# Kernel tuning notes

Measured on AMD Instinct MI355X. Metric: run time of the kernel, lower is better.

The kernel has to match this reference:

```python
import jax, jax.numpy as jnp
import numpy as np

N, P, D, C = 2048, 64, 512, 32   # bs*n_vars, patch_num, hidden_dim, cluster_num
H, DFF, L = 8, 2048, 3           # heads, ffn dim, encoder layers
TEMP = 10.0
EPS = 1e-10
LN_EPS = 1e-5


def setup_inputs() -> dict:
    key = jax.random.key(0)
    ks = jax.random.split(key, 18)
    s = 0.02  # small init to keep activations sane
    inp = {}
    inp["input_series"] = jax.random.normal(ks[0], (N, P, D), jnp.float32)
    pi = jax.random.uniform(ks[1], (C,), jnp.float32) + 0.1
    inp["text_pi"] = pi / pi.sum()
    A = jax.random.uniform(ks[2], (C, C), jnp.float32) + 0.1
    inp["text_A"] = A / A.sum(axis=1, keepdims=True)
    # stacked per-layer TransformerEncoderLayer params (torch post-norm, relu)
    inp["qkv_w"] = jax.random.normal(ks[3], (L, 3 * D, D), jnp.float32) * s
    inp["qkv_b"] = jnp.zeros((L, 3 * D), jnp.float32)
    inp["out_w"] = jax.random.normal(ks[4], (L, D, D), jnp.float32) * s
    inp["out_b"] = jnp.zeros((L, D), jnp.float32)
    inp["ln1_w"] = jnp.ones((L, D), jnp.float32)
    inp["ln1_b"] = jnp.zeros((L, D), jnp.float32)
    inp["ff1_w"] = jax.random.normal(ks[5], (L, DFF, D), jnp.float32) * s
    inp["ff1_b"] = jnp.zeros((L, DFF), jnp.float32)
    inp["ff2_w"] = jax.random.normal(ks[6], (L, D, DFF), jnp.float32) * s
    inp["ff2_b"] = jnp.zeros((L, D), jnp.float32)
    inp["ln2_w"] = jnp.ones((L, D), jnp.float32)
    inp["ln2_b"] = jnp.zeros((L, D), jnp.float32)
    inp["mus"] = jax.random.normal(ks[7], (C, D), jnp.float32)
    return inp


def _layer_norm(x, w, b):
    m = x.mean(axis=-1, keepdims=True)
    v = ((x - m) ** 2).mean(axis=-1, keepdims=True)
    return (x - m) * jax.lax.rsqrt(v + LN_EPS) * w + b


def _encoder_layer(x, qkv_w, qkv_b, out_w, out_b, ln1_w, ln1_b,
                   ff1_w, ff1_b, ff2_w, ff2_b, ln2_w, ln2_b):
    n, p, d = x.shape
    dh = d // H
    qkv = x @ qkv_w.T + qkv_b                       # [n,p,3d]
    q, k, v = jnp.split(qkv, 3, axis=-1)
    def split_heads(t):
        return t.reshape(n, p, H, dh).transpose(0, 2, 1, 3)  # [n,h,p,dh]
    q, k, v = split_heads(q), split_heads(k), split_heads(v)
    scores = jnp.einsum('nhqd,nhkd->nhqk', q, k) / (dh ** 0.5)
    attn = jax.nn.softmax(scores, axis=-1)
    o = jnp.einsum('nhqk,nhkd->nhqd', attn, v)
    o = o.transpose(0, 2, 1, 3).reshape(n, p, d)
    o = o @ out_w.T + out_b
    x = _layer_norm(x + o, ln1_w, ln1_b)            # post-norm
    f = jax.nn.relu(x @ ff1_w.T + ff1_b) @ ff2_w.T + ff2_b
    return _layer_norm(x + f, ln2_w, ln2_b)


def reference(input_series, text_pi, text_A, qkv_w, qkv_b, out_w, out_b,
              ln1_w, ln1_b, ff1_w, ff1_b, ff2_w, ff2_b, ln2_w, ln2_b, mus):
    x = input_series
    for l in range(L):
        x = _encoder_layer(x, qkv_w[l], qkv_b[l], out_w[l], out_b[l],
                           ln1_w[l], ln1_b[l], ff1_w[l], ff1_b[l],
                           ff2_w[l], ff2_b[l], ln2_w[l], ln2_b[l])
    emb_ts = x                                       # [N,P,D]
    # ClusterCenters: softmax of exp(-||x - tanh(mu)||^2 / T)
    mu = jnp.tanh(mus)                               # [C,D]
    dist = ((emb_ts ** 2).sum(-1)[..., None]
            + (mu ** 2).sum(-1)[None, None, :]
            - 2.0 * jnp.einsum('npd,cd->npc', emb_ts, mu))  # [N,P,C]
    z = jnp.exp(-dist / TEMP)
    logits_all = z / z.sum(axis=-1, keepdims=True)
    log_za = jnp.log(logits_all + EPS)               # [N,P,C]
    # sequential HMM-style recursion over patches
    l0 = jax.nn.softmax(jnp.log(text_pi + EPS)[None, :] + log_za[:, 0], axis=-1)
    def step(c, lz):
        c2 = jax.nn.softmax(jnp.log(c @ text_A + EPS) + lz, axis=-1)
        return c2, c2
    _, ys = jax.lax.scan(step, l0, jnp.swapaxes(log_za[:, 1:], 0, 1))  # [P-1,N,C]
    cluster_probs = jnp.concatenate([l0[:, None], jnp.swapaxes(ys, 0, 1)], axis=1)
    entropy_loss = -jnp.sum(cluster_probs * jnp.log(cluster_probs + EPS), axis=-1).mean()
    return (cluster_probs, emb_ts, text_pi, text_A, entropy_loss)
```

## Files before the change

kernel.cpp:

```cpp
#include <hip/hip_runtime.h>
#include <stdint.h>


typedef __bf16 bf16;
typedef __bf16 bf16x2 __attribute__((ext_vector_type(2)));
typedef __bf16 bf16x4 __attribute__((ext_vector_type(4)));
typedef __bf16 bf16x8 __attribute__((ext_vector_type(8)));
typedef float  f32x4  __attribute__((ext_vector_type(4)));
typedef float  f32x2  __attribute__((ext_vector_type(2)));

#define EPSF 1e-10f
#define NROWS 131072L

__device__ __forceinline__ float bflo(uint32_t u){ return __uint_as_float(u << 16); }
__device__ __forceinline__ float bfhi(uint32_t u){ return __uint_as_float(u & 0xffff0000u); }

__device__ __forceinline__ void gload_lds16(const bf16* g, bf16* l){
  __builtin_amdgcn_global_load_lds((const __attribute__((address_space(1))) uint32_t*)g,
                                   (__attribute__((address_space(3))) uint32_t*)l,
                                   16, 0, 0);
}

__global__ void k_f2bf(const float* __restrict__ in, bf16* __restrict__ out, long n){
  const long stride = (long)gridDim.x * blockDim.x * 4;
  for (long i = ((long)blockIdx.x * blockDim.x + threadIdx.x) * 4; i < n; i += stride){
    f32x4 v = *(const f32x4*)(in + i);
    bf16x4 o = { (bf16)v[0], (bf16)v[1], (bf16)v[2], (bf16)v[3] };
    *(bf16x4*)(out + i) = o;
  }
}

__global__ void k_bf2f(const bf16* __restrict__ in, float* __restrict__ out, long n){
  const long stride = (long)gridDim.x * blockDim.x * 4;
  for (long i = ((long)blockIdx.x * blockDim.x + threadIdx.x) * 4; i < n; i += stride){
    bf16x4 v = *(const bf16x4*)(in + i);
    f32x4 o = { (float)v[0], (float)v[1], (float)v[2], (float)v[3] };
    *(f32x4*)(out + i) = o;
  }
}


#define MFMA_PH(RH, CH)                                                       \
  {                                                                           \
    __builtin_amdgcn_s_setprio(1);                                            \
    _Pragma("unroll")                                                         \
    for (int i2 = 0; i2 < 4; i2++) {                                          \
      _Pragma("unroll")                                                       \
      for (int j2 = 0; j2 < 2; j2++) {                                        \
        acc[(RH)*4+i2][(CH)*2+j2] = __builtin_amdgcn_mfma_f32_16x16x32_bf16(  \
            a[i2][0], b[CH][j2][0], acc[(RH)*4+i2][(CH)*2+j2], 0, 0, 0);      \
        acc[(RH)*4+i2][(CH)*2+j2] = __builtin_amdgcn_mfma_f32_16x16x32_bf16(  \
            a[i2][1], b[CH][j2][1], acc[(RH)*4+i2][(CH)*2+j2], 0, 0, 0);      \
      }                                                                       \
    }                                                                         \
    __builtin_amdgcn_s_setprio(0);                                            \
  }

#define RD_A(RH)                                                              \
  _Pragma("unroll")                                                           \
  for (int i2 = 0; i2 < 4; i2++) {                                            \
    a[i2][0] = *(const bf16x8*)&Ac[(aRow + (RH)*64 + i2*16) * 64 + sl0];      \
    a[i2][1] = *(const bf16x8*)&Ac[(aRow + (RH)*64 + i2*16) * 64 + sl1];      \
  }

#define RD_B(CH)                                                              \
  _Pragma("unroll")                                                           \
  for (int j2 = 0; j2 < 2; j2++) {                                            \
    b[CH][j2][0] = *(const bf16x8*)&Bc[(bRow + (CH)*32 + j2*16) * 64 + sl0];  \
    b[CH][j2][1] = *(const bf16x8*)&Bc[(bRow + (CH)*32 + j2*16) * 64 + sl1];  \
  }

#define ISSUE_A(dst, BI, KK) \
  gload_lds16(gA + (long)(BI)*64*lda + (KK), (dst) + (BI)*4096 + wslice)
#define ISSUE_B(dst, BI, KK) \
  gload_lds16(gB + (long)(BI)*64*K   + (KK), (dst) + (BI)*4096 + wslice)

#define WAITV(N)  asm volatile("s_waitcnt vmcnt(" #N ")" ::: "memory")
#define WAITL0    asm volatile("s_waitcnt lgkmcnt(0)" ::: "memory")
#define BARRIER   { __builtin_amdgcn_s_barrier(); asm volatile("" ::: "memory"); }

template<int RELU>
__global__ __launch_bounds__(512, 2)
void gemm256(const bf16* __restrict__ A, long lda,
             const bf16* __restrict__ W,
             const float* __restrict__ bias,
             bf16* __restrict__ Cb, long K, int nbx)
{
  const int tid  = threadIdx.x;
  const int wid  = tid >> 6;
  const int lane = tid & 63;
  const int wr = wid >> 2, wc = wid & 3;
  const long ldc = (long)nbx * 256;

  const unsigned nwg = gridDim.x;
  const unsigned q   = nwg >> 3;
  const unsigned swz = (blockIdx.x & 7) * q + (blockIdx.x >> 3);
  const unsigned bx  = swz % (unsigned)nbx;
  const unsigned by  = swz / (unsigned)nbx;
  const long bm = (long)by * 256;
  const long bn = (long)bx * 256;

  __shared__ __align__(16) bf16 smem[65536];
  bf16* const As0 = smem;
  bf16* const Bs0 = smem + 16384;
  bf16* const As1 = smem + 32768;
  bf16* const Bs1 = smem + 49152;

  const int srow   = wid * 8 + (lane >> 3);
  const int scol   = ((lane & 7) ^ ((lane >> 3) & 7)) * 8;
  const int wslice = wid * 512;
  const bf16* gA = A + (bm + srow) * lda + scol;
  const bf16* gB = W + (bn + srow) * K   + scol;

  const int fr = lane & 15, fg = lane >> 4;
  const int aRow = wr * 128 + fr;
  const int bRow = wc * 64  + fr;
  const int sl0 = ((0 + fg) ^ (fr & 7)) * 8;
  const int sl1 = ((4 + fg) ^ (fr & 7)) * 8;

  f32x4 acc[8][4];
#pragma unroll
  for (int i = 0; i < 8; i++)
#pragma unroll
    for (int j = 0; j < 4; j++) acc[i][j] = (f32x4){0.f, 0.f, 0.f, 0.f};

  bf16x8 a[4][2];
  bf16x8 b[2][2][2];

  const int nt = (int)(K >> 6);

  ISSUE_A(As0, 0, 0); ISSUE_A(As0, 2, 0);
  ISSUE_B(Bs0, 0, 0); ISSUE_B(Bs0, 1, 0);
  ISSUE_B(Bs0, 2, 0); ISSUE_B(Bs0, 3, 0);
  ISSUE_A(As0, 1, 0); ISSUE_A(As0, 3, 0);
  WAITV(2);
  BARRIER;

  for (int t = 0; t < nt; t++){
    bf16* const Ac = (t & 1) ? As1 : As0;
    bf16* const Bc = (t & 1) ? Bs1 : Bs0;
    bf16* const An = (t & 1) ? As0 : As1;
    bf16* const Bn = (t & 1) ? Bs0 : Bs1;
    const bool stage = (t + 1 < nt);
    const long kn = (long)(t + 1) << 6;

    RD_A(0); RD_B(0);
    if (stage){ ISSUE_A(An, 0, kn); ISSUE_A(An, 2, kn);
                ISSUE_B(Bn, 0, kn); ISSUE_B(Bn, 1, kn); }
    BARRIER;
    WAITL0;
    MFMA_PH(0, 0);
    BARRIER;

    RD_B(1);
    if (stage){ ISSUE_B(Bn, 2, kn); ISSUE_B(Bn, 3, kn); WAITV(6); }
    else      { WAITV(0); }
    BARRIER;
    WAITL0;
    MFMA_PH(0, 1);
    BARRIER;

    RD_A(1);
    if (stage){ ISSUE_A(An, 1, kn); ISSUE_A(An, 3, kn); }
    BARRIER;
    WAITL0;
    MFMA_PH(1, 0);
    BARRIER;

    WAITV(2);
    BARRIER;
    MFMA_PH(1, 1);
    BARRIER;
  }

#pragma unroll
  for (int j = 0; j < 4; j++){
    const long col = bn + wc * 64 + j * 16 + fr;
    const float bv = bias[col];
#pragma unroll
    for (int i = 0; i < 8; i++){
#pragma unroll
      for (int r = 0; r < 4; r++){
        const long row = bm + wr * 128 + i * 16 + fg * 4 + r;
        float v = acc[i][j][r] + bv;
        if (RELU) v = fmaxf(v, 0.f);
        Cb[row * ldc + col] = (bf16)v;
      }
    }
  }
}

__global__ __launch_bounds__(256)
void attention(bf16* __restrict__ qkv)
{
  const int blk = blockIdx.x;
  const long n = blk >> 3;
  const int h  = blk & 7;
  const int tid = threadIdx.x;
  const int wid = tid >> 6, lane = tid & 63;

  __shared__ __align__(16) bf16 Qs[64][72];
  __shared__ __align__(16) bf16 Ks[64][72];
  __shared__ __align__(16) bf16 Vt[64][72];

  bf16* base = qkv + n * 64 * 1536 + h * 64;

  for (int c = tid; c < 512; c += 256){
    const int row = c >> 3, col = (c & 7) * 8;
    const long go = (long)row * 1536 + col;
    *(bf16x8*)&Qs[row][col] = *(const bf16x8*)(base + go);
    *(bf16x8*)&Ks[row][col] = *(const bf16x8*)(base + 512 + go);
    bf16x8 v = *(const bf16x8*)(base + 1024 + go);
#pragma unroll
    for (int e = 0; e < 8; e++) Vt[col + e][row] = v[e];
  }
  __syncthreads();

  const int fr = lane & 15, fg = lane >> 4;
  f32x4 sacc[4];
#pragma unroll
  for (int j = 0; j < 4; j++) sacc[j] = (f32x4){0.f, 0.f, 0.f, 0.f};
#pragma unroll
  for (int ks = 0; ks < 2; ks++){
    bf16x8 aa = *(const bf16x8*)&Qs[wid * 16 + fr][ks * 32 + fg * 8];
#pragma unroll
    for (int j = 0; j < 4; j++){
      bf16x8 bb = *(const bf16x8*)&Ks[j * 16 + fr][ks * 32 + fg * 8];
      sacc[j] = __builtin_amdgcn_mfma_f32_16x16x32_bf16(aa, bb, sacc[j], 0, 0, 0);
    }
  }

  float pv[4][4];
#pragma unroll
  for (int r = 0; r < 4; r++){
    float m = -1e30f;
#pragma unroll
    for (int j = 0; j < 4; j++) m = fmaxf(m, sacc[j][r]);
#pragma unroll
    for (int msk = 1; msk < 16; msk <<= 1) m = fmaxf(m, __shfl_xor(m, msk));
    float s = 0.f;
#pragma unroll
    for (int j = 0; j < 4; j++){
      float p = __expf((sacc[j][r] - m) * 0.125f);
      pv[j][r] = p; s += p;
    }
#pragma unroll
    for (int msk = 1; msk < 16; msk <<= 1) s += __shfl_xor(s, msk);
    const float inv = 1.f / s;
#pragma unroll
    for (int j = 0; j < 4; j++) pv[j][r] *= inv;
  }

#pragma unroll
  for (int j = 0; j < 4; j++)
#pragma unroll
    for (int r = 0; r < 4; r++)
      Qs[wid * 16 + fg * 4 + r][j * 16 + fr] = (bf16)pv[j][r];
  __syncthreads();

  f32x4 oacc[4];
#pragma unroll
  for (int j = 0; j < 4; j++) oacc[j] = (f32x4){0.f, 0.f, 0.f, 0.f};
#pragma unroll
  for (int ks = 0; ks < 2; ks++){
    bf16x8 aa = *(const bf16x8*)&Qs[wid * 16 + fr][ks * 32 + fg * 8];
#pragma unroll
    for (int j = 0; j < 4; j++){
      bf16x8 bb = *(const bf16x8*)&Vt[j * 16 + fr][ks * 32 + fg * 8];
      oacc[j] = __builtin_amdgcn_mfma_f32_16x16x32_bf16(aa, bb, oacc[j], 0, 0, 0);
    }
  }
#pragma unroll
  for (int j = 0; j < 4; j++)
#pragma unroll
    for (int r = 0; r < 4; r++)
      base[(long)(wid * 16 + fg * 4 + r) * 1536 + j * 16 + fr] = (bf16)oacc[j][r];
}

__global__ __launch_bounds__(256)
void resid_ln(const bf16* __restrict__ X, const bf16* __restrict__ O,
              const float* __restrict__ w, const float* __restrict__ b,
              bf16* __restrict__ Y)
{
  const long row = blockIdx.x;
  const int tid = threadIdx.x, lane = tid & 63, wid = tid >> 6;
  const uint32_t xu = ((const uint32_t*)(X + row * 512))[tid];
  const uint32_t ou = ((const uint32_t*)(O + row * 512))[tid];
  const float s0 = bflo(xu) + bflo(ou);
  const float s1 = bfhi(xu) + bfhi(ou);
  float sum = s0 + s1, sq = s0 * s0 + s1 * s1;
#pragma unroll
  for (int m = 1; m < 64; m <<= 1){ sum += __shfl_xor(sum, m); sq += __shfl_xor(sq, m); }
  __shared__ float red[8];
  if (lane == 0){ red[wid] = sum; red[4 + wid] = sq; }
  __syncthreads();
  sum = red[0] + red[1] + red[2] + red[3];
  sq  = red[4] + red[5] + red[6] + red[7];
  const float mean = sum * (1.f / 512.f);
  const float var  = sq * (1.f / 512.f) - mean * mean;
  const float rs   = rsqrtf(var + 1e-5f);
  const f32x2 wv = *(const f32x2*)(w + 2 * tid);
  const f32x2 bv = *(const f32x2*)(b + 2 * tid);
  bf16x2 o2 = { (bf16)((s0 - mean) * rs * wv[0] + bv[0]),
                (bf16)((s1 - mean) * rs * wv[1] + bv[1]) };
  *(bf16x2*)(Y + row * 512 + 2 * tid) = o2;
}

__global__ __launch_bounds__(256)
void k_mu(const float* __restrict__ mus, bf16* __restrict__ mubf, float* __restrict__ munorm)
{
  const int c = blockIdx.x, tid = threadIdx.x, lane = tid & 63, wid = tid >> 6;
  const f32x2 v = *(const f32x2*)(mus + c * 512 + 2 * tid);
  const float t0 = tanhf(v[0]), t1 = tanhf(v[1]);
  bf16x2 o2 = { (bf16)t0, (bf16)t1 };
  *(bf16x2*)(mubf + c * 512 + 2 * tid) = o2;
  float sq = t0 * t0 + t1 * t1;
#pragma unroll
  for (int m = 1; m < 64; m <<= 1) sq += __shfl_xor(sq, m);
  __shared__ float red[4];
  if (lane == 0) red[wid] = sq;
  __syncthreads();
  if (tid == 0) munorm[c] = red[0] + red[1] + red[2] + red[3];
}

__global__ __launch_bounds__(256)
void cluster_logza(const bf16* __restrict__ X, const bf16* __restrict__ MU,
                   const float* __restrict__ munorm, float* __restrict__ out)
{
  const int tid = threadIdx.x, lane = tid & 63, wid = tid >> 6;
  __shared__ __align__(16) bf16 mus[32][512];
  __shared__ float xs[512];
  __shared__ float red[4];
  __shared__ float dots[32];
  for (int c = tid; c < 2048; c += 256){
    const int r = c >> 6, col = (c & 63) * 8;
    *(bf16x8*)&mus[r][col] = *(const bf16x8*)(MU + r * 512 + col);
  }
  const int cc = tid >> 3, seg = tid & 7;
  const long row0 = (long)blockIdx.x * 16;
  __syncthreads();
  for (int rr = 0; rr < 16; rr++){
    const long row = row0 + rr;
    const uint32_t u = ((const uint32_t*)(X + row * 512))[tid];
    const float aa = bflo(u), bb = bfhi(u);
    xs[2 * tid] = aa; xs[2 * tid + 1] = bb;
    float sq = aa * aa + bb * bb;
#pragma unroll
    for (int m = 1; m < 64; m <<= 1) sq += __shfl_xor(sq, m);
    if (lane == 0) red[wid] = sq;
    __syncthreads();
    const float xn = red[0] + red[1] + red[2] + red[3];
    float p = 0.f;
#pragma unroll
    for (int jj = 0; jj < 8; jj++){
      const int col = jj * 64 + seg * 8;
      bf16x8 m8 = *(const bf16x8*)&mus[cc][col];
      const float* xv = &xs[col];
#pragma unroll
      for (int e = 0; e < 8; e++) p += xv[e] * (float)m8[e];
    }
#pragma unroll
    for (int m = 1; m < 8; m <<= 1) p += __shfl_xor(p, m);
    if (seg == 0) dots[cc] = p;
    __syncthreads();
    if (tid < 32){
      const float dist = xn + munorm[tid] - 2.f * dots[tid];
      const float lg = -dist * 0.1f;
      float mx = lg;
#pragma unroll
      for (int m = 1; m < 32; m <<= 1) mx = fmaxf(mx, __shfl_xor(mx, m, 32));
      const float z = __expf(lg - mx);
      float s = z;
#pragma unroll
      for (int m = 1; m < 32; m <<= 1) s += __shfl_xor(s, m, 32);
      out[row * 32 + tid] = logf(z / s + EPSF);
    }
    __syncthreads();
  }
}

__global__ __launch_bounds__(256)
void k_hmm(const float* __restrict__ lza, const float* __restrict__ pi,
           const float* __restrict__ A, float* __restrict__ cp, float* __restrict__ ent)
{
  __shared__ float As[32][33];
  const int tid = threadIdx.x;
  for (int i = tid; i < 1024; i += 256) As[i >> 5][i & 31] = A[i];
  __syncthreads();
  const int j = tid & 31;
  const long n = (long)blockIdx.x * 8 + (tid >> 5);
  const float* lz = lza + n * 2048;

  float c = logf(pi[j] + EPSF) + lz[j];
  {
    float mx = c;
#pragma unroll
    for (int m = 1; m < 32; m <<= 1) mx = fmaxf(mx, __shfl_xor(mx, m, 32));
    float z = __expf(c - mx), s = z;
#pragma unroll
    for (int m = 1; m < 32; m <<= 1) s += __shfl_xor(s, m, 32);
    c = z / s;
  }
  cp[n * 2048 + j] = c;
  float ea = -c * logf(c + EPSF);

  for (int p = 1; p < 64; p++){
    float y = 0.f;
#pragma unroll
    for (int i = 0; i < 32; i++) y += __shfl(c, i, 32) * As[i][j];
    float t = logf(y + EPSF) + lz[p * 32 + j];
    float mx = t;
#pragma unroll
    for (int m = 1; m < 32; m <<= 1) mx = fmaxf(mx, __shfl_xor(mx, m, 32));
    float z = __expf(t - mx), s = z;
#pragma unroll
    for (int m = 1; m < 32; m <<= 1) s += __shfl_xor(s, m, 32);
    c = z / s;
    cp[n * 2048 + p * 32 + j] = c;
    ea += -c * logf(c + EPSF);
  }
#pragma unroll
  for (int m = 1; m < 32; m <<= 1) ea += __shfl_xor(ea, m, 32);
  if (j == 0) atomicAdd(ent, ea * (1.f / 131072.f));
}

extern "C" void kernel_launch(void* const* d_in, const int* in_sizes, int n_in,
                              void* d_out, int out_size, void* d_ws, size_t ws_size,
                              hipStream_t stream)
{
  (void)in_sizes; (void)n_in; (void)out_size; (void)ws_size;
  const float* in_series = (const float*)d_in[0];
  const float* pi    = (const float*)d_in[1];
  const float* Amat  = (const float*)d_in[2];
  const float* qkv_w = (const float*)d_in[3];
  const float* qkv_b = (const float*)d_in[4];
  const float* out_w = (const float*)d_in[5];
  const float* out_b = (const float*)d_in[6];
  const float* ln1_w = (const float*)d_in[7];
  const float* ln1_b = (const float*)d_in[8];
  const float* ff1_w = (const float*)d_in[9];
  const float* ff1_b = (const float*)d_in[10];
  const float* ff2_w = (const float*)d_in[11];
  const float* ff2_b = (const float*)d_in[12];
  const float* ln2_w = (const float*)d_in[13];
  const float* ln2_b = (const float*)d_in[14];
  const float* mus   = (const float*)d_in[15];

  char* ws = (char*)d_ws;
  bf16* region0 = (bf16*)(ws);
  bf16* xb      = (bf16*)(ws + 536870912L);
  bf16* oproj   = (bf16*)(ws + 671088640L);
  bf16* w_qkv   = (bf16*)(ws + 805306368L);
  bf16* w_out   = (bf16*)(ws + 810024960L);
  bf16* w_ff1   = (bf16*)(ws + 811597824L);
  bf16* w_ff2   = (bf16*)(ws + 817889280L);
  bf16* mubf    = (bf16*)(ws + 824180736L);
  float* munorm = (float*)(ws + 824213504L);
  float* logza  = (float*)(ws);

  float* out_f = (float*)d_out;
  float* cp    = out_f;
  float* emb   = out_f + 4194304L;
  float* o_pi  = out_f + 71303168L;
  float* o_A   = out_f + 71303200L;
  float* o_ent = out_f + 71304224L;

  k_f2bf<<<8192, 256, 0, stream>>>(in_series, xb, 67108864L);
  k_f2bf<<<1024, 256, 0, stream>>>(qkv_w, w_qkv, 2359296L);
  k_f2bf<<<1024, 256, 0, stream>>>(out_w, w_out, 786432L);
  k_f2bf<<<1024, 256, 0, stream>>>(ff1_w, w_ff1, 3145728L);
  k_f2bf<<<1024, 256, 0, stream>>>(ff2_w, w_ff2, 3145728L);
  k_mu<<<32, 256, 0, stream>>>(mus, mubf, munorm);

  for (int l = 0; l < 3; l++){
    gemm256<0><<<3072, 512, 0, stream>>>(xb, 512, w_qkv + (long)l * 786432L,
                                         qkv_b + (long)l * 1536, region0, 512, 6);
    attention<<<16384, 256, 0, stream>>>(region0);
    gemm256<0><<<1024, 512, 0, stream>>>(region0, 1536, w_out + (long)l * 262144L,
                                         out_b + (long)l * 512, oproj, 512, 2);
    resid_ln<<<131072, 256, 0, stream>>>(xb, oproj, ln1_w + (long)l * 512, ln1_b + (long)l * 512, xb);
    gemm256<1><<<4096, 512, 0, stream>>>(xb, 512, w_ff1 + (long)l * 1048576L,
                                         ff1_b + (long)l * 2048, region0, 512, 8);
    gemm256<0><<<1024, 512, 0, stream>>>(region0, 2048, w_ff2 + (long)l * 1048576L,
                                         ff2_b + (long)l * 512, oproj, 2048, 2);
    resid_ln<<<131072, 256, 0, stream>>>(xb, oproj, ln2_w + (long)l * 512, ln2_b + (long)l * 512, xb);
  }

  k_bf2f<<<8192, 256, 0, stream>>>(xb, emb, 67108864L);
  cluster_logza<<<8192, 256, 0, stream>>>(xb, mubf, munorm, logza);
  hipMemsetAsync(o_ent, 0, 4, stream);
  k_hmm<<<256, 256, 0, stream>>>(logza, pi, Amat, cp, o_ent);
  hipMemcpyAsync(o_pi, pi, 32 * sizeof(float), hipMemcpyDeviceToDevice, stream);
  hipMemcpyAsync(o_A, Amat, 1024 * sizeof(float), hipMemcpyDeviceToDevice, stream);
}
```

Before: 4.835 ms.

## Stage GEMM epilogue through LDS, widen LayerNorm rows, fuse final fp32 emit

The GEMM epilogue now writes accumulators with bias and ReLU into a per-wave LDS buffer, then reads them back as rows and stores 16-byte bf16x8 vectors instead of scattered 2-byte stores. resid_ln processes one row per wave with 16-byte loads and no block-level shared reduction. The last LN also writes the fp32 embedding output, which removes the separate bf16-to-fp32 conversion kernel. The costs are extra LDS traffic and reuse of the GEMM shared memory, and the fp32 embedding is now taken before bf16 rounding.

```diff
diff --git a/kernel.cpp b/kernel.cpp
--- a/kernel.cpp
+++ b/kernel.cpp
@@ -27,15 +27,6 @@
     f32x4 v = *(const f32x4*)(in + i);
     bf16x4 o = { (bf16)v[0], (bf16)v[1], (bf16)v[2], (bf16)v[3] };
     *(bf16x4*)(out + i) = o;
-  }
-}
-
-__global__ void k_bf2f(const bf16* __restrict__ in, float* __restrict__ out, long n){
-  const long stride = (long)gridDim.x * blockDim.x * 4;
-  for (long i = ((long)blockIdx.x * blockDim.x + threadIdx.x) * 4; i < n; i += stride){
-    bf16x4 v = *(const bf16x4*)(in + i);
-    f32x4 o = { (float)v[0], (float)v[1], (float)v[2], (float)v[3] };
-    *(f32x4*)(out + i) = o;
   }
 }
 
@@ -173,20 +164,41 @@
     BARRIER;
   }
 
-#pragma unroll
-  for (int j = 0; j < 4; j++){
-    const long col = bn + wc * 64 + j * 16 + fr;
-    const float bv = bias[col];
-#pragma unroll
-    for (int i = 0; i < 8; i++){
-#pragma unroll
-      for (int r = 0; r < 4; r++){
-        const long row = bm + wr * 128 + i * 16 + fg * 4 + r;
-        float v = acc[i][j][r] + bv;
-        if (RELU) v = fmaxf(v, 0.f);
-        Cb[row * ldc + col] = (bf16)v;
+  float* const cw = (float*)smem + wid * 2176;
+  const long strip_row0 = bm + wr * 128;
+  const long strip_col0 = bn + wc * 64;
+  float bv[4];
+#pragma unroll
+  for (int j = 0; j < 4; j++) bv[j] = bias[strip_col0 + j * 16 + fr];
+  const int rrow = lane >> 3;
+  const int rcol = (lane & 7) * 8;
+
+#pragma unroll
+  for (int ch = 0; ch < 4; ch++){
+#pragma unroll
+    for (int i2 = 0; i2 < 2; i2++){
+      const int i = ch * 2 + i2;
+#pragma unroll
+      for (int j = 0; j < 4; j++){
+#pragma unroll
+        for (int r = 0; r < 4; r++){
+          float v = acc[i][j][r] + bv[j];
+          if (RELU) v = fmaxf(v, 0.f);
+          cw[(i2 * 16 + fg * 4 + r) * 68 + j * 16 + fr] = v;
+        }
       }
     }
+    WAITL0;
+#pragma unroll
+    for (int p = 0; p < 4; p++){
+      const int row = p * 8 + rrow;
+      f32x4 v0 = *(const f32x4*)&cw[row * 68 + rcol];
+      f32x4 v1 = *(const f32x4*)&cw[row * 68 + rcol + 4];
+      bf16x8 o = { (bf16)v0[0], (bf16)v0[1], (bf16)v0[2], (bf16)v0[3],
+                   (bf16)v1[0], (bf16)v1[1], (bf16)v1[2], (bf16)v1[3] };
+      *(bf16x8*)&Cb[(strip_row0 + ch * 32 + row) * ldc + strip_col0 + rcol] = o;
+    }
+    WAITL0;
   }
 }
 
@@ -280,30 +292,43 @@
 __global__ __launch_bounds__(256)
 void resid_ln(const bf16* __restrict__ X, const bf16* __restrict__ O,
               const float* __restrict__ w, const float* __restrict__ b,
-              bf16* __restrict__ Y)
-{
-  const long row = blockIdx.x;
-  const int tid = threadIdx.x, lane = tid & 63, wid = tid >> 6;
-  const uint32_t xu = ((const uint32_t*)(X + row * 512))[tid];
-  const uint32_t ou = ((const uint32_t*)(O + row * 512))[tid];
-  const float s0 = bflo(xu) + bflo(ou);
-  const float s1 = bfhi(xu) + bfhi(ou);
-  float sum = s0 + s1, sq = s0 * s0 + s1 * s1;
+              bf16* __restrict__ Y, float* __restrict__ EF)
+{
+  const int wid = threadIdx.x >> 6, lane = threadIdx.x & 63;
+  const long row = (long)blockIdx.x * 4 + wid;
+  const uint4 xu = ((const uint4*)(X + row * 512))[lane];
+  const uint4 ou = ((const uint4*)(O + row * 512))[lane];
+  float s[8];
+  s[0] = bflo(xu.x) + bflo(ou.x);  s[1] = bfhi(xu.x) + bfhi(ou.x);
+  s[2] = bflo(xu.y) + bflo(ou.y);  s[3] = bfhi(xu.y) + bfhi(ou.y);
+  s[4] = bflo(xu.z) + bflo(ou.z);  s[5] = bfhi(xu.z) + bfhi(ou.z);
+  s[6] = bflo(xu.w) + bflo(ou.w);  s[7] = bfhi(xu.w) + bfhi(ou.w);
+  float sum = 0.f, sq = 0.f;
+#pragma unroll
+  for (int e = 0; e < 8; e++){ sum += s[e]; sq += s[e] * s[e]; }
 #pragma unroll
   for (int m = 1; m < 64; m <<= 1){ sum += __shfl_xor(sum, m); sq += __shfl_xor(sq, m); }
-  __shared__ float red[8];
-  if (lane == 0){ red[wid] = sum; red[4 + wid] = sq; }
-  __syncthreads();
-  sum = red[0] + red[1] + red[2] + red[3];
-  sq  = red[4] + red[5] + red[6] + red[7];
   const float mean = sum * (1.f / 512.f);
   const float var  = sq * (1.f / 512.f) - mean * mean;
   const float rs   = rsqrtf(var + 1e-5f);
-  const f32x2 wv = *(const f32x2*)(w + 2 * tid);
-  const f32x2 bv = *(const f32x2*)(b + 2 * tid);
-  bf16x2 o2 = { (bf16)((s0 - mean) * rs * wv[0] + bv[0]),
-                (bf16)((s1 - mean) * rs * wv[1] + bv[1]) };
-  *(bf16x2*)(Y + row * 512 + 2 * tid) = o2;
+  const f32x4 w0 = *(const f32x4*)(w + 8 * lane);
+  const f32x4 w1 = *(const f32x4*)(w + 8 * lane + 4);
+  const f32x4 b0 = *(const f32x4*)(b + 8 * lane);
+  const f32x4 b1 = *(const f32x4*)(b + 8 * lane + 4);
+  float o[8];
+#pragma unroll
+  for (int e = 0; e < 4; e++) o[e]     = (s[e]     - mean) * rs * w0[e] + b0[e];
+#pragma unroll
+  for (int e = 0; e < 4; e++) o[e + 4] = (s[e + 4] - mean) * rs * w1[e] + b1[e];
+  bf16x8 ov = { (bf16)o[0], (bf16)o[1], (bf16)o[2], (bf16)o[3],
+                (bf16)o[4], (bf16)o[5], (bf16)o[6], (bf16)o[7] };
+  *(bf16x8*)(Y + row * 512 + 8 * lane) = ov;
+  if (EF){
+    f32x4 e0 = { o[0], o[1], o[2], o[3] };
+    f32x4 e1 = { o[4], o[5], o[6], o[7] };
+    *(f32x4*)(EF + row * 512 + 8 * lane) = e0;
+    *(f32x4*)(EF + row * 512 + 8 * lane + 4) = e1;
+  }
 }
 
 __global__ __launch_bounds__(256)
@@ -478,15 +503,17 @@
     attention<<<16384, 256, 0, stream>>>(region0);
     gemm256<0><<<1024, 512, 0, stream>>>(region0, 1536, w_out + (long)l * 262144L,
                                          out_b + (long)l * 512, oproj, 512, 2);
-    resid_ln<<<131072, 256, 0, stream>>>(xb, oproj, ln1_w + (long)l * 512, ln1_b + (long)l * 512, xb);
+    resid_ln<<<32768, 256, 0, stream>>>(xb, oproj, ln1_w + (long)l * 512,
+                                        ln1_b + (long)l * 512, xb, nullptr);
     gemm256<1><<<4096, 512, 0, stream>>>(xb, 512, w_ff1 + (long)l * 1048576L,
                                          ff1_b + (long)l * 2048, region0, 512, 8);
     gemm256<0><<<1024, 512, 0, stream>>>(region0, 2048, w_ff2 + (long)l * 1048576L,
                                          ff2_b + (long)l * 512, oproj, 2048, 2);
-    resid_ln<<<131072, 256, 0, stream>>>(xb, oproj, ln2_w + (long)l * 512, ln2_b + (long)l * 512, xb);
-  }
-
-  k_bf2f<<<8192, 256, 0, stream>>>(xb, emb, 67108864L);
+    resid_ln<<<32768, 256, 0, stream>>>(xb, oproj, ln2_w + (long)l * 512,
+                                        ln2_b + (long)l * 512, xb,
+                                        (l == 2) ? emb : nullptr);
+  }
+
   cluster_logza<<<8192, 256, 0, stream>>>(xb, mubf, munorm, logza);
   hipMemsetAsync(o_ent, 0, 4, stream);
   k_hmm<<<256, 256, 0, stream>>>(logza, pi, Amat, cp, o_ent);
```

New measurement: 4.031 ms. 16.6% less time.
